# Optimization experiments

Measured on AMD Instinct MI355X. Metric: run time of the kernel, lower is better.

Reference implementation:

```python
import jax, jax.numpy as jnp
import numpy as np

N, D, DFF, H, L = 98280, 192, 384, 8, 36
S = N // L  # 2730 sets per partition
HD = D // H
EPS = 1e-5


def _ln(x, g, b):
    m = x.mean(-1, keepdims=True)
    v = ((x - m) ** 2).mean(-1, keepdims=True)
    return (x - m) * jax.lax.rsqrt(v + EPS) * g + b


def _mha(q, k, v, Wqkv, bqkv, Wo, bo, mask):
    # q,k,v: (S, L, D); mask: (S, L), True = padded key
    Wq, Wk, Wv = jnp.split(Wqkv, 3, axis=0)
    bq, bk, bv = jnp.split(bqkv, 3)
    qh = (q @ Wq.T + bq).reshape(S, L, H, HD)
    kh = (k @ Wk.T + bk).reshape(S, L, H, HD)
    vh = (v @ Wv.T + bv).reshape(S, L, H, HD)
    scores = jnp.einsum('slhd,smhd->shlm', qh, kh) / np.sqrt(HD).astype(np.float32)
    scores = jnp.where(mask[:, None, None, :], -1e9, scores)
    attn = jax.nn.softmax(scores, axis=-1)
    out = jnp.einsum('shlm,smhd->slhd', attn, vh).reshape(S, L, D)
    return out @ Wo.T + bo


def _layer(x, pos, inds, mask, Wqkv, bqkv, Wo, bo, W1, b1, W2, b2,
           g1, be1, g2, be2, gn, bn):
    identity = x
    sf = x[inds]                 # gather voxels into sets: (S, L, D)
    qk = sf + pos[inds]          # pos added to q and k only (value = sf)
    src2 = _mha(qk, qk, sf, Wqkv, bqkv, Wo, bo, mask)
    flat = inds.reshape(-1)
    # torch.unique(return_inverse) + flip + scatter == take FIRST occurrence
    # of each voxel id; .at[].min is deterministic under duplicates.
    perm = jnp.full((N,), flat.shape[0], jnp.int32).at[flat].min(
        jnp.arange(flat.shape[0], dtype=jnp.int32))
    src2 = src2.reshape(-1, D)[perm]   # scatter back: (N, D)
    x = _ln(x + src2, g1, be1)
    ff = jnp.maximum(x @ W1.T + b1, 0.0) @ W2.T + b2
    x = _ln(x + ff, g2, be2)
    return _ln(x + identity, gn, bn)   # DSVT_EncoderLayer residual norm


def reference(src, inds0, inds1, mask0, mask1, pos0, pos1,
              Wqkv, bqkv, Wo, bo, W1, b1, W2, b2,
              g1, be1, g2, be2, gn, bn, block_id):
    inds = (inds0, inds1)
    masks = (mask0, mask1)
    pos = (pos0, pos1)
    out = src
    for i in range(2):  # two set partitions within the shift (shift_id = block_id % 2)
        out = _layer(out, pos[i], inds[i], masks[i],
                     Wqkv[i], bqkv[i], Wo[i], bo[i],
                     W1[i], b1[i], W2[i], b2[i],
                     g1[i], be1[i], g2[i], be2[i], gn[i], bn[i])
    return out


def setup_inputs():
    key = jax.random.key(0)
    ks = jax.random.split(key, 16)
    sd = 0.02
    return {
        "src": jax.random.normal(ks[0], (N, D), jnp.float32),
        "inds0": jax.random.permutation(ks[1], N).reshape(S, L).astype(jnp.int32),
        "inds1": jax.random.permutation(ks[2], N).reshape(S, L).astype(jnp.int32),
        "mask0": jnp.zeros((S, L), bool),
        "mask1": jnp.zeros((S, L), bool),
        "pos0": jax.random.normal(ks[3], (N, D), jnp.float32),
        "pos1": jax.random.normal(ks[4], (N, D), jnp.float32),
        "Wqkv": sd * jax.random.normal(ks[5], (2, 3 * D, D), jnp.float32),
        "bqkv": jnp.zeros((2, 3 * D), jnp.float32),
        "Wo": sd * jax.random.normal(ks[6], (2, D, D), jnp.float32),
        "bo": jnp.zeros((2, D), jnp.float32),
        "W1": sd * jax.random.normal(ks[7], (2, DFF, D), jnp.float32),
        "b1": jnp.zeros((2, DFF), jnp.float32),
        "W2": sd * jax.random.normal(ks[8], (2, D, DFF), jnp.float32),
        "b2": jnp.zeros((2, D), jnp.float32),
        "g1": jnp.ones((2, D), jnp.float32),
        "be1": jnp.zeros((2, D), jnp.float32),
        "g2": jnp.ones((2, D), jnp.float32),
        "be2": jnp.zeros((2, D), jnp.float32),
        "gn": jnp.ones((2, D), jnp.float32),
        "bn": jnp.zeros((2, D), jnp.float32),
        "block_id": 0,
    }
```

## Files before the change

### kernel.cpp

```cpp
#include <hip/hip_runtime.h>
#include <stdint.h>

#define NVOX   98280
#define S_SETS 2730
#define L_SET  36
#define D_MODEL 192
#define D_FF    384
#define N_HEADS 8
#define H_DIM   24

using s16x8 = __attribute__((ext_vector_type(8))) short;
using s16x4 = __attribute__((ext_vector_type(4))) short;
using f32x4 = __attribute__((ext_vector_type(4))) float;

__device__ __forceinline__ float bf2f(unsigned short h) {
    unsigned u = ((unsigned)h) << 16;
    return __builtin_bit_cast(float, u);
}
__device__ __forceinline__ unsigned short f2bf(float f) {
    unsigned u = __builtin_bit_cast(unsigned, f);
    u += 0x7FFF + ((u >> 16) & 1);
    return (unsigned short)(u >> 16);
}

__global__ __launch_bounds__(256)
void convert_f32_bf16(const float* __restrict__ src, short* __restrict__ dst, int n)
{
    int i = blockIdx.x * 256 + threadIdx.x;
    if (i < n) dst[i] = (short)f2bf(src[i]);
}

__global__ __launch_bounds__(256)
void gather_kernel(const float* __restrict__ x, const float* __restrict__ pos,
                   const int* __restrict__ inds,
                   short* __restrict__ qk, short* __restrict__ sf)
{
    int f = blockIdx.x * 4 + (threadIdx.x >> 6);
    int lane = threadIdx.x & 63;
    if (lane >= 48) return;
    int v = inds[f];
    float4 a = *(const float4*)(x + (size_t)v * D_MODEL + lane * 4);
    float4 p = *(const float4*)(pos + (size_t)v * D_MODEL + lane * 4);
    s16x4 q, s;
    q[0] = (short)f2bf(a.x + p.x); q[1] = (short)f2bf(a.y + p.y);
    q[2] = (short)f2bf(a.z + p.z); q[3] = (short)f2bf(a.w + p.w);
    s[0] = (short)f2bf(a.x); s[1] = (short)f2bf(a.y);
    s[2] = (short)f2bf(a.z); s[3] = (short)f2bf(a.w);
    *(s16x4*)(qk + (size_t)f * D_MODEL + lane * 4) = q;
    *(s16x4*)(sf + (size_t)f * D_MODEL + lane * 4) = s;
}

__global__ __launch_bounds__(512, 4)
void qkv_direct(const short* __restrict__ qk, const short* __restrict__ sf,
                const short* __restrict__ W, const float* __restrict__ bias,
                short* __restrict__ C, int n)
{
    __shared__ char Bs[36864];
    const int bx = blockIdx.x;
    const int sec = bx >> 1, half = bx & 1;
    const int colOff = sec * 192 + half * 96;
    const short* Ap = (sec == 2) ? sf : qk;
    const short* Wp = W + (size_t)colOff * 192;
    const int rowBase = blockIdx.y * 128;
    const int tid = threadIdx.x;

    #pragma unroll
    for (int t = tid; t < 2304; t += 512) {
        int row = t / 24, c8 = t % 24;
        s16x8 v = *(const s16x8*)(Wp + (size_t)row * 192 + c8 * 8);
        *(s16x8*)(Bs + row * 384 + ((c8 * 16) ^ ((row & 7) << 4))) = v;
    }
    __syncthreads();

    const int wid = tid >> 6, lane = tid & 63;
    const int lr = lane & 15, kb = lane >> 4;
    const int arow = rowBase + wid * 16 + lr;
    const bool rv = arow < n;
    const short* Arow = Ap + (size_t)arow * 192 + kb * 8;

    f32x4 acc[6] = {};
    #pragma unroll
    for (int ks = 0; ks < 6; ++ks) {
        s16x8 a = {};
        if (rv) a = *(const s16x8*)(Arow + ks * 32);
        s16x8 b[6];
        #pragma unroll
        for (int fj = 0; fj < 6; ++fj) {
            int row = fj * 16 + lr;
            b[fj] = *(const s16x8*)(Bs + row * 384 + ((ks * 64 + kb * 16) ^ ((row & 7) << 4)));
        }
        #pragma unroll
        for (int fj = 0; fj < 6; ++fj)
            acc[fj] = __builtin_amdgcn_mfma_f32_16x16x32_bf16(a, b[fj], acc[fj], 0, 0, 0);
    }
    #pragma unroll
    for (int fj = 0; fj < 6; ++fj) {
        int col = colOff + fj * 16 + lr;
        float bv = bias[col];
        #pragma unroll
        for (int r = 0; r < 4; ++r) {
            int grow = rowBase + wid * 16 + kb * 4 + r;
            if (grow < n)
                C[(size_t)grow * 576 + col] = (short)f2bf(acc[fj][r] + bv);
        }
    }
}

__global__ __launch_bounds__(64)
void attn_mfma(const short* __restrict__ qkv, const unsigned char* __restrict__ mask,
               short* __restrict__ attn_out)
{
    const int s = blockIdx.x >> 3;
    const int h = blockIdx.x & 7;
    __shared__ short Pl[48 * 64];
    __shared__ short Vt[32 * 64];
    char* Pb = (char*)Pl;
    char* Vb = (char*)Vt;
    const int lane = threadIdx.x;
    const int lr = lane & 15, g = lane >> 4;

    #pragma unroll
    for (int i = 0; i < 6; ++i)
        *(s16x8*)(Pl + i * 512 + lane * 8) = (s16x8){};
    #pragma unroll
    for (int i = 0; i < 4; ++i)
        *(s16x8*)(Vt + i * 512 + lane * 8) = (s16x8){};
    if (lane < L_SET) {
        const short* vrow = qkv + (size_t)(s * L_SET + lane) * 576 + 384 + h * H_DIM;
        #pragma unroll
        for (int j = 0; j < 3; ++j) {
            s16x8 v = *(const s16x8*)(vrow + j * 8);
            #pragma unroll
            for (int e = 0; e < 8; ++e) {
                int d = j * 8 + e;
                *(short*)(Vb + d * 128 + ((lane * 2) ^ ((d & 7) << 4))) = v[e];
            }
        }
    }

    s16x8 qa[3], kb[3];
    #pragma unroll
    for (int t = 0; t < 3; ++t) {
        int rr = t * 16 + lr;
        qa[t] = (s16x8){};
        kb[t] = (s16x8){};
        if (rr < L_SET && g < 3) {
            const short* base = qkv + (size_t)(s * L_SET + rr) * 576 + h * H_DIM + g * 8;
            qa[t] = *(const s16x8*)(base);
            kb[t] = *(const s16x8*)(base + 192);
        }
    }
    f32x4 sc[3][3] = {};
    #pragma unroll
    for (int mt = 0; mt < 3; ++mt)
        #pragma unroll
        for (int nt = 0; nt < 3; ++nt)
            sc[mt][nt] = __builtin_amdgcn_mfma_f32_16x16x32_bf16(qa[mt], kb[nt], sc[mt][nt], 0, 0, 0);

    const float scale = 0.20412414523193154f;
    bool colmask[3];
    #pragma unroll
    for (int nt = 0; nt < 3; ++nt) {
        int m = nt * 16 + lr;
        colmask[nt] = (m >= L_SET) || (mask[(size_t)s * L_SET + (m < L_SET ? m : 0)] != 0);
    }
    #pragma unroll
    for (int mt = 0; mt < 3; ++mt) {
        #pragma unroll
        for (int r = 0; r < 4; ++r) {
            float v[3], ev[3];
            #pragma unroll
            for (int nt = 0; nt < 3; ++nt)
                v[nt] = colmask[nt] ? -1e9f : sc[mt][nt][r] * scale;
            float mx = fmaxf(fmaxf(v[0], v[1]), v[2]);
            #pragma unroll
            for (int off = 1; off < 16; off <<= 1) mx = fmaxf(mx, __shfl_xor(mx, off, 64));
            float sm = 0.f;
            #pragma unroll
            for (int nt = 0; nt < 3; ++nt) { ev[nt] = __expf(v[nt] - mx); sm += ev[nt]; }
            #pragma unroll
            for (int off = 1; off < 16; off <<= 1) sm += __shfl_xor(sm, off, 64);
            float rinv = 1.f / sm;
            int q = mt * 16 + g * 4 + r;
            #pragma unroll
            for (int nt = 0; nt < 3; ++nt) {
                int m = nt * 16 + lr;
                *(short*)(Pb + q * 128 + ((m * 2) ^ ((q & 7) << 4))) =
                    (short)f2bf(ev[nt] * rinv);
            }
        }
    }

    f32x4 o[3][2] = {};
    #pragma unroll
    for (int ks = 0; ks < 2; ++ks) {
        s16x8 pa[3], vb[2];
        #pragma unroll
        for (int mt = 0; mt < 3; ++mt) {
            int row = mt * 16 + lr;
            pa[mt] = *(const s16x8*)(Pb + row * 128 + ((ks * 64 + g * 16) ^ ((row & 7) << 4)));
        }
        #pragma unroll
        for (int nt = 0; nt < 2; ++nt) {
            int row = nt * 16 + lr;
            vb[nt] = *(const s16x8*)(Vb + row * 128 + ((ks * 64 + g * 16) ^ ((row & 7) << 4)));
        }
        #pragma unroll
        for (int mt = 0; mt < 3; ++mt)
            #pragma unroll
            for (int nt = 0; nt < 2; ++nt)
                o[mt][nt] = __builtin_amdgcn_mfma_f32_16x16x32_bf16(pa[mt], vb[nt], o[mt][nt], 0, 0, 0);
    }

    #pragma unroll
    for (int mt = 0; mt < 3; ++mt) {
        #pragma unroll
        for (int nt = 0; nt < 2; ++nt) {
            #pragma unroll
            for (int r = 0; r < 4; ++r) {
                int q = mt * 16 + g * 4 + r;
                int d = nt * 16 + lr;
                if (q < L_SET && d < H_DIM)
                    attn_out[(size_t)(s * L_SET + q) * D_MODEL + h * H_DIM + d] =
                        (short)f2bf(o[mt][nt][r]);
            }
        }
    }
}

__device__ __forceinline__ float wave_sum64(float v) {
    #pragma unroll
    for (int off = 32; off > 0; off >>= 1) v += __shfl_xor(v, off, 64);
    return v;
}

__global__ __launch_bounds__(512)
void wo_ln1(const short* __restrict__ attnb, const short* __restrict__ Wo,
            const float* __restrict__ bo, const int* __restrict__ inds,
            const float* __restrict__ xin,
            const float* __restrict__ g1, const float* __restrict__ be1,
            short* __restrict__ x1, int n)
{
    extern __shared__ char pool[];
    char* As = pool;
    char* Bs = pool + 49152;
    float* Cf = (float*)pool;
    const int rowBase = blockIdx.x * 128;
    const int tid = threadIdx.x;

    #pragma unroll
    for (int t = tid; t < 3072; t += 512) {
        int row = t / 24, c8 = t % 24;
        int grow = rowBase + row;
        s16x8 v = {};
        if (grow < n) v = *(const s16x8*)(attnb + (size_t)grow * 192 + c8 * 8);
        *(s16x8*)(As + row * 384 + ((c8 * 16) ^ ((row & 7) << 4))) = v;
    }
    #pragma unroll
    for (int t = tid; t < 4608; t += 512) {
        int row = t / 24, c8 = t % 24;
        s16x8 v = *(const s16x8*)(Wo + (size_t)row * 192 + c8 * 8);
        *(s16x8*)(Bs + row * 384 + ((c8 * 16) ^ ((row & 7) << 4))) = v;
    }
    __syncthreads();

    const int wid = tid >> 6, lane = tid & 63;
    const int lr = lane & 15, kb = lane >> 4;
    const int wm = wid & 3, wn = wid >> 2;
    f32x4 acc[2][6] = {};
    #pragma unroll
    for (int ks = 0; ks < 6; ++ks) {
        s16x8 a[2], b[6];
        #pragma unroll
        for (int fi = 0; fi < 2; ++fi) {
            int row = wm * 32 + fi * 16 + lr;
            a[fi] = *(const s16x8*)(As + row * 384 + ((ks * 64 + kb * 16) ^ ((row & 7) << 4)));
        }
        #pragma unroll
        for (int fj = 0; fj < 6; ++fj) {
            int row = wn * 96 + fj * 16 + lr;
            b[fj] = *(const s16x8*)(Bs + row * 384 + ((ks * 64 + kb * 16) ^ ((row & 7) << 4)));
        }
        #pragma unroll
        for (int fi = 0; fi < 2; ++fi)
            #pragma unroll
            for (int fj = 0; fj < 6; ++fj)
                acc[fi][fj] = __builtin_amdgcn_mfma_f32_16x16x32_bf16(a[fi], b[fj], acc[fi][fj], 0, 0, 0);
    }
    __syncthreads();
    #pragma unroll
    for (int fj = 0; fj < 6; ++fj) {
        int col = wn * 96 + fj * 16 + lr;
        float bv = bo[col];
        #pragma unroll
        for (int fi = 0; fi < 2; ++fi)
            #pragma unroll
            for (int r = 0; r < 4; ++r) {
                int row = wm * 32 + fi * 16 + kb * 4 + r;
                Cf[row * 192 + col] = acc[fi][fj][r] + bv;
            }
    }
    __syncthreads();

    int vv[16];
    #pragma unroll
    for (int i = 0; i < 16; ++i) {
        int f = rowBase + wid * 16 + i;
        vv[i] = (f < n) ? inds[f] : 0;
    }
    float4 xr[16];
    #pragma unroll
    for (int i = 0; i < 16; ++i)
        xr[i] = (lane < 48) ? *(const float4*)(xin + (size_t)vv[i] * D_MODEL + lane * 4)
                            : make_float4(0.f, 0.f, 0.f, 0.f);
    float4 gv = (lane < 48) ? *(const float4*)(g1 + lane * 4) : make_float4(0,0,0,0);
    float4 bv = (lane < 48) ? *(const float4*)(be1 + lane * 4) : make_float4(0,0,0,0);
    #pragma unroll
    for (int i = 0; i < 16; ++i) {
        int r = wid * 16 + i;
        int f = rowBase + r;
        float4 t = make_float4(0.f, 0.f, 0.f, 0.f);
        if (lane < 48) {
            float4 c4 = *(const float4*)&Cf[r * 192 + lane * 4];
            t.x = c4.x + xr[i].x; t.y = c4.y + xr[i].y;
            t.z = c4.z + xr[i].z; t.w = c4.w + xr[i].w;
        }
        float mean = wave_sum64(t.x + t.y + t.z + t.w) * (1.f / 192.f);
        float ss   = wave_sum64(t.x*t.x + t.y*t.y + t.z*t.z + t.w*t.w) * (1.f / 192.f);
        float inv = rsqrtf(ss - mean * mean + 1e-5f);
        if (lane < 48 && f < n) {
            s16x4 o;
            o[0] = (short)f2bf((t.x - mean) * inv * gv.x + bv.x);
            o[1] = (short)f2bf((t.y - mean) * inv * gv.y + bv.y);
            o[2] = (short)f2bf((t.z - mean) * inv * gv.z + bv.z);
            o[3] = (short)f2bf((t.w - mean) * inv * gv.w + bv.w);
            *(s16x4*)(x1 + (size_t)vv[i] * D_MODEL + lane * 4) = o;
        }
    }
}

__global__ __launch_bounds__(512)
void ffn_fused(const short* __restrict__ x1, const short* __restrict__ W1,
               const float* __restrict__ b1, const short* __restrict__ W2,
               const float* __restrict__ b2, const float* __restrict__ xin,
               const float* __restrict__ g2, const float* __restrict__ be2,
               const float* __restrict__ gn, const float* __restrict__ bn,
               float* __restrict__ outp, int n)
{
    extern __shared__ char pool[];
    char* Ax  = pool;
    char* W1c = pool + 49152;
    char* W2c = pool + 86016;
    char* Hc  = pool + 125952;
    float* Cf = (float*)(pool + 49152);
    const int rowBase = blockIdx.x * 128;
    const int tid = threadIdx.x;
    const int wid = tid >> 6, lane = tid & 63;
    const int lr = lane & 15, kb = lane >> 4;
    const int wm = wid & 3, wn = wid >> 2;

    #pragma unroll
    for (int t = tid; t < 3072; t += 512) {
        int row = t / 24, c8 = t % 24;
        int grow = rowBase + row;
        s16x8 v = {};
        if (grow < n) v = *(const s16x8*)(x1 + (size_t)grow * 192 + c8 * 8);
        *(s16x8*)(Ax + row * 384 + ((c8 * 16) ^ ((row & 7) << 4))) = v;
    }

    f32x4 acc2[2][6] = {};
    for (int c = 0; c < 4; ++c) {
        __syncthreads();
        #pragma unroll
        for (int t = tid; t < 2304; t += 512) {
            int row = t / 24, c8 = t % 24;
            s16x8 v = *(const s16x8*)(W1 + (size_t)(c * 96 + row) * 192 + c8 * 8);
            *(s16x8*)(W1c + row * 384 + ((c8 * 16) ^ ((row & 7) << 4))) = v;
        }
        #pragma unroll
        for (int t = tid; t < 2304; t += 512) {
            int row = t / 12, c8 = t % 12;
            s16x8 v = *(const s16x8*)(W2 + (size_t)row * 384 + c * 96 + c8 * 8);
            *(s16x8*)(W2c + row * 208 + c8 * 16) = v;
        }
        __syncthreads();
        f32x4 acc1[2][3] = {};
        #pragma unroll
        for (int ks = 0; ks < 6; ++ks) {
            s16x8 a[2], b[3];
            #pragma unroll
            for (int fi = 0; fi < 2; ++fi) {
                int row = wm * 32 + fi * 16 + lr;
                a[fi] = *(const s16x8*)(Ax + row * 384 + ((ks * 64 + kb * 16) ^ ((row & 7) << 4)));
            }
            #pragma unroll
            for (int fj = 0; fj < 3; ++fj) {
                int row = wn * 48 + fj * 16 + lr;
                b[fj] = *(const s16x8*)(W1c + row * 384 + ((ks * 64 + kb * 16) ^ ((row & 7) << 4)));
            }
            #pragma unroll
            for (int fi = 0; fi < 2; ++fi)
                #pragma unroll
                for (int fj = 0; fj < 3; ++fj)
                    acc1[fi][fj] = __builtin_amdgcn_mfma_f32_16x16x32_bf16(a[fi], b[fj], acc1[fi][fj], 0, 0, 0);
        }
        #pragma unroll
        for (int fj = 0; fj < 3; ++fj) {
            int col = wn * 48 + fj * 16 + lr;
            float b1v = b1[c * 96 + col];
            #pragma unroll
            for (int fi = 0; fi < 2; ++fi)
                #pragma unroll
                for (int r = 0; r < 4; ++r) {
                    int row = wm * 32 + fi * 16 + kb * 4 + r;
                    *(short*)(Hc + row * 208 + col * 2) =
                        (short)f2bf(fmaxf(acc1[fi][fj][r] + b1v, 0.f));
                }
        }
        __syncthreads();
        #pragma unroll
        for (int ks = 0; ks < 3; ++ks) {
            s16x8 a[2], b[6];
            #pragma unroll
            for (int fi = 0; fi < 2; ++fi) {
                int row = wm * 32 + fi * 16 + lr;
                a[fi] = *(const s16x8*)(Hc + row * 208 + ks * 64 + kb * 16);
            }
            #pragma unroll
            for (int fj = 0; fj < 6; ++fj) {
                int row = wn * 96 + fj * 16 + lr;
                b[fj] = *(const s16x8*)(W2c + row * 208 + ks * 64 + kb * 16);
            }
            #pragma unroll
            for (int fi = 0; fi < 2; ++fi)
                #pragma unroll
                for (int fj = 0; fj < 6; ++fj)
                    acc2[fi][fj] = __builtin_amdgcn_mfma_f32_16x16x32_bf16(a[fi], b[fj], acc2[fi][fj], 0, 0, 0);
        }
    }
    __syncthreads();
    #pragma unroll
    for (int fj = 0; fj < 6; ++fj) {
        int col = wn * 96 + fj * 16 + lr;
        float bv = b2[col];
        #pragma unroll
        for (int fi = 0; fi < 2; ++fi)
            #pragma unroll
            for (int r = 0; r < 4; ++r) {
                int row = wm * 32 + fi * 16 + kb * 4 + r;
                Cf[row * 192 + col] = acc2[fi][fj][r] + bv;
            }
    }
    __syncthreads();

    float4 xr[16];
    #pragma unroll
    for (int i = 0; i < 16; ++i) {
        int gvx = rowBase + wid * 16 + i;
        xr[i] = (lane < 48 && gvx < n)
              ? *(const float4*)(xin + (size_t)gvx * D_MODEL + lane * 4)
              : make_float4(0.f, 0.f, 0.f, 0.f);
    }
    float4 g2v = (lane < 48) ? *(const float4*)(g2 + lane * 4) : make_float4(0,0,0,0);
    float4 b2v = (lane < 48) ? *(const float4*)(be2 + lane * 4) : make_float4(0,0,0,0);
    float4 gnv = (lane < 48) ? *(const float4*)(gn + lane * 4) : make_float4(0,0,0,0);
    float4 bnv = (lane < 48) ? *(const float4*)(bn + lane * 4) : make_float4(0,0,0,0);
    #pragma unroll
    for (int i = 0; i < 16; ++i) {
        int r = wid * 16 + i;
        int gvx = rowBase + r;
        float4 t = make_float4(0.f, 0.f, 0.f, 0.f);
        if (lane < 48) {
            float4 f4 = *(const float4*)&Cf[r * 192 + lane * 4];
            int byteoff = r * 384 + (((lane >> 1) << 4) ^ ((r & 7) << 4)) + ((lane & 1) << 3);
            s16x4 xv = *(const s16x4*)(Ax + byteoff);
            t.x = f4.x + bf2f((unsigned short)xv[0]);
            t.y = f4.y + bf2f((unsigned short)xv[1]);
            t.z = f4.z + bf2f((unsigned short)xv[2]);
            t.w = f4.w + bf2f((unsigned short)xv[3]);
        }
        float m1 = wave_sum64(t.x + t.y + t.z + t.w) * (1.f / 192.f);
        float s1 = wave_sum64(t.x*t.x + t.y*t.y + t.z*t.z + t.w*t.w) * (1.f / 192.f);
        float i1 = rsqrtf(s1 - m1 * m1 + 1e-5f);
        float4 t2 = make_float4(0.f, 0.f, 0.f, 0.f);
        if (lane < 48) {
            t2.x = (t.x - m1) * i1 * g2v.x + b2v.x + xr[i].x;
            t2.y = (t.y - m1) * i1 * g2v.y + b2v.y + xr[i].y;
            t2.z = (t.z - m1) * i1 * g2v.z + b2v.z + xr[i].z;
            t2.w = (t.w - m1) * i1 * g2v.w + b2v.w + xr[i].w;
        }
        float m2 = wave_sum64(t2.x + t2.y + t2.z + t2.w) * (1.f / 192.f);
        float s2 = wave_sum64(t2.x*t2.x + t2.y*t2.y + t2.z*t2.z + t2.w*t2.w) * (1.f / 192.f);
        float i2 = rsqrtf(s2 - m2 * m2 + 1e-5f);
        if (lane < 48 && gvx < n) {
            float4 o;
            o.x = (t2.x - m2) * i2 * gnv.x + bnv.x;
            o.y = (t2.y - m2) * i2 * gnv.y + bnv.y;
            o.z = (t2.z - m2) * i2 * gnv.z + bnv.z;
            o.w = (t2.w - m2) * i2 * gnv.w + bnv.w;
            *(float4*)(outp + (size_t)gvx * D_MODEL + lane * 4) = o;
        }
    }
}

extern "C" void kernel_launch(void* const* d_in, const int* in_sizes, int n_in,
                              void* d_out, int out_size, void* d_ws, size_t ws_size,
                              hipStream_t stream)
{
    (void)in_sizes; (void)n_in; (void)out_size;
    const int N = NVOX;
    const float* src = (const float*)d_in[0];
    const int* inds[2] = {(const int*)d_in[1], (const int*)d_in[2]};
    const unsigned char* mask[2] = {(const unsigned char*)d_in[3], (const unsigned char*)d_in[4]};
    const float* pos[2] = {(const float*)d_in[5], (const float*)d_in[6]};
    const float* Wqkv = (const float*)d_in[7];
    const float* bqkv = (const float*)d_in[8];
    const float* Wo   = (const float*)d_in[9];
    const float* bo   = (const float*)d_in[10];
    const float* W1   = (const float*)d_in[11];
    const float* b1   = (const float*)d_in[12];
    const float* W2   = (const float*)d_in[13];
    const float* b2   = (const float*)d_in[14];
    const float* g1   = (const float*)d_in[15];
    const float* be1  = (const float*)d_in[16];
    const float* g2   = (const float*)d_in[17];
    const float* be2  = (const float*)d_in[18];
    const float* gn   = (const float*)d_in[19];
    const float* bn   = (const float*)d_in[20];

    float* out = (float*)d_out;
    short* wsS = (short*)d_ws;

    const size_t NE = (size_t)N * D_MODEL;
    short* wqkv_b = wsS;
    short* wo_b   = wsS + 221184;
    short* w1_b   = wsS + 294912;
    short* w2_b   = wsS + 442368;
    const size_t base = 1048576;
    short* qk    = wsS + base;
    short* sf    = qk + NE;
    short* qkvb  = sf + NE;
    short* attnb = qkvb + 3 * NE;
    short* x1    = attnb + NE;

    if (ws_size < (base + 7 * NE) * sizeof(short)) return;

    const dim3 blk(256);
    convert_f32_bf16<<<dim3(864), blk, 0, stream>>>(Wqkv, wqkv_b, 221184);
    convert_f32_bf16<<<dim3(288), blk, 0, stream>>>(Wo,   wo_b,   73728);
    convert_f32_bf16<<<dim3(576), blk, 0, stream>>>(W1,   w1_b,   147456);
    convert_f32_bf16<<<dim3(576), blk, 0, stream>>>(W2,   w2_b,   147456);

    const int RT = (N + 127) / 128;
    for (int i = 0; i < 2; ++i) {
        const float* xin = (i == 0) ? src : out;
        gather_kernel<<<dim3(24570), blk, 0, stream>>>(xin, pos[i], inds[i], qk, sf);
        qkv_direct<<<dim3(6, RT), dim3(512), 0, stream>>>(
            qk, sf, wqkv_b + (size_t)i * 110592, bqkv + i * 576, qkvb, N);
        attn_mfma<<<dim3(S_SETS * N_HEADS), dim3(64), 0, stream>>>(qkvb, mask[i], attnb);
        wo_ln1<<<dim3(RT), dim3(512), 122880, stream>>>(
            attnb, wo_b + (size_t)i * 36864, bo + i * 192, inds[i], xin,
            g1 + i * 192, be1 + i * 192, x1, N);
        ffn_fused<<<dim3(RT), dim3(512), 152576, stream>>>(
            x1, w1_b + (size_t)i * 73728, b1 + i * 384, w2_b + (size_t)i * 73728,
            b2 + i * 192, xin, g2 + i * 192, be2 + i * 192,
            gn + i * 192, bn + i * 192, out, N);
    }
}
```

Measured before the change: 790.1 us.

## Restructure Wo+LN1 and FFN kernels so each wave owns full output rows

Both post-attention kernels are rewritten to use 256-thread blocks in which each wave computes all 192 output columns for 32 rows. Weights are read straight from global memory (relying on cache) instead of being staged in LDS, and the A tile for Wo is also read directly. LayerNorm runs on the MFMA accumulators in registers with 16-lane shuffle reductions, removing the LDS round trip and several barriers. In exchange it raises register pressure (24 accumulator tiles plus temporaries), issues many narrow scalar global loads and stores for the residual and outputs, and re-reads weights per wave.

```diff
diff --git a/kernel.cpp b/kernel.cpp
--- a/kernel.cpp
+++ b/kernel.cpp
@@ -228,277 +228,210 @@
     }
 }
 
-__device__ __forceinline__ float wave_sum64(float v) {
-    #pragma unroll
-    for (int off = 32; off > 0; off >>= 1) v += __shfl_xor(v, off, 64);
-    return v;
-}
-
-__global__ __launch_bounds__(512)
-void wo_ln1(const short* __restrict__ attnb, const short* __restrict__ Wo,
-            const float* __restrict__ bo, const int* __restrict__ inds,
-            const float* __restrict__ xin,
-            const float* __restrict__ g1, const float* __restrict__ be1,
-            short* __restrict__ x1, int n)
-{
-    extern __shared__ char pool[];
-    char* As = pool;
-    char* Bs = pool + 49152;
-    float* Cf = (float*)pool;
+__global__ __launch_bounds__(256)
+void wo_wave(const short* __restrict__ attnb, const short* __restrict__ Wo,
+             const float* __restrict__ bo, const int* __restrict__ inds,
+             const float* __restrict__ xin,
+             const float* __restrict__ g1, const float* __restrict__ be1,
+             short* __restrict__ x1, int n)
+{
     const int rowBase = blockIdx.x * 128;
     const int tid = threadIdx.x;
-
-    #pragma unroll
-    for (int t = tid; t < 3072; t += 512) {
-        int row = t / 24, c8 = t % 24;
-        int grow = rowBase + row;
-        s16x8 v = {};
-        if (grow < n) v = *(const s16x8*)(attnb + (size_t)grow * 192 + c8 * 8);
-        *(s16x8*)(As + row * 384 + ((c8 * 16) ^ ((row & 7) << 4))) = v;
-    }
-    #pragma unroll
-    for (int t = tid; t < 4608; t += 512) {
-        int row = t / 24, c8 = t % 24;
-        s16x8 v = *(const s16x8*)(Wo + (size_t)row * 192 + c8 * 8);
-        *(s16x8*)(Bs + row * 384 + ((c8 * 16) ^ ((row & 7) << 4))) = v;
-    }
-    __syncthreads();
-
-    const int wid = tid >> 6, lane = tid & 63;
+    const int w = tid >> 6, lane = tid & 63;
     const int lr = lane & 15, kb = lane >> 4;
-    const int wm = wid & 3, wn = wid >> 2;
-    f32x4 acc[2][6] = {};
+
+    f32x4 acc[2][12] = {};
     #pragma unroll
     for (int ks = 0; ks < 6; ++ks) {
-        s16x8 a[2], b[6];
+        s16x8 a[2], b[12];
         #pragma unroll
         for (int fi = 0; fi < 2; ++fi) {
-            int row = wm * 32 + fi * 16 + lr;
-            a[fi] = *(const s16x8*)(As + row * 384 + ((ks * 64 + kb * 16) ^ ((row & 7) << 4)));
-        }
-        #pragma unroll
-        for (int fj = 0; fj < 6; ++fj) {
-            int row = wn * 96 + fj * 16 + lr;
-            b[fj] = *(const s16x8*)(Bs + row * 384 + ((ks * 64 + kb * 16) ^ ((row & 7) << 4)));
-        }
+            int arow = rowBase + w * 32 + fi * 16 + lr;
+            a[fi] = (s16x8){};
+            if (arow < n)
+                a[fi] = *(const s16x8*)(attnb + (size_t)arow * 192 + ks * 32 + kb * 8);
+        }
+        #pragma unroll
+        for (int fj = 0; fj < 12; ++fj)
+            b[fj] = *(const s16x8*)(Wo + (size_t)(fj * 16 + lr) * 192 + ks * 32 + kb * 8);
         #pragma unroll
         for (int fi = 0; fi < 2; ++fi)
             #pragma unroll
-            for (int fj = 0; fj < 6; ++fj)
+            for (int fj = 0; fj < 12; ++fj)
                 acc[fi][fj] = __builtin_amdgcn_mfma_f32_16x16x32_bf16(a[fi], b[fj], acc[fi][fj], 0, 0, 0);
     }
-    __syncthreads();
-    #pragma unroll
-    for (int fj = 0; fj < 6; ++fj) {
-        int col = wn * 96 + fj * 16 + lr;
-        float bv = bo[col];
-        #pragma unroll
-        for (int fi = 0; fi < 2; ++fi)
-            #pragma unroll
-            for (int r = 0; r < 4; ++r) {
-                int row = wm * 32 + fi * 16 + kb * 4 + r;
-                Cf[row * 192 + col] = acc[fi][fj][r] + bv;
-            }
-    }
-    __syncthreads();
-
-    int vv[16];
-    #pragma unroll
-    for (int i = 0; i < 16; ++i) {
-        int f = rowBase + wid * 16 + i;
-        vv[i] = (f < n) ? inds[f] : 0;
-    }
-    float4 xr[16];
-    #pragma unroll
-    for (int i = 0; i < 16; ++i)
-        xr[i] = (lane < 48) ? *(const float4*)(xin + (size_t)vv[i] * D_MODEL + lane * 4)
-                            : make_float4(0.f, 0.f, 0.f, 0.f);
-    float4 gv = (lane < 48) ? *(const float4*)(g1 + lane * 4) : make_float4(0,0,0,0);
-    float4 bv = (lane < 48) ? *(const float4*)(be1 + lane * 4) : make_float4(0,0,0,0);
-    #pragma unroll
-    for (int i = 0; i < 16; ++i) {
-        int r = wid * 16 + i;
-        int f = rowBase + r;
-        float4 t = make_float4(0.f, 0.f, 0.f, 0.f);
-        if (lane < 48) {
-            float4 c4 = *(const float4*)&Cf[r * 192 + lane * 4];
-            t.x = c4.x + xr[i].x; t.y = c4.y + xr[i].y;
-            t.z = c4.z + xr[i].z; t.w = c4.w + xr[i].w;
-        }
-        float mean = wave_sum64(t.x + t.y + t.z + t.w) * (1.f / 192.f);
-        float ss   = wave_sum64(t.x*t.x + t.y*t.y + t.z*t.z + t.w*t.w) * (1.f / 192.f);
-        float inv = rsqrtf(ss - mean * mean + 1e-5f);
-        if (lane < 48 && f < n) {
-            s16x4 o;
-            o[0] = (short)f2bf((t.x - mean) * inv * gv.x + bv.x);
-            o[1] = (short)f2bf((t.y - mean) * inv * gv.y + bv.y);
-            o[2] = (short)f2bf((t.z - mean) * inv * gv.z + bv.z);
-            o[3] = (short)f2bf((t.w - mean) * inv * gv.w + bv.w);
-            *(s16x4*)(x1 + (size_t)vv[i] * D_MODEL + lane * 4) = o;
-        }
-    }
-}
-
-__global__ __launch_bounds__(512)
-void ffn_fused(const short* __restrict__ x1, const short* __restrict__ W1,
-               const float* __restrict__ b1, const short* __restrict__ W2,
-               const float* __restrict__ b2, const float* __restrict__ xin,
-               const float* __restrict__ g2, const float* __restrict__ be2,
-               const float* __restrict__ gn, const float* __restrict__ bn,
-               float* __restrict__ outp, int n)
-{
-    extern __shared__ char pool[];
-    char* Ax  = pool;
-    char* W1c = pool + 49152;
-    char* W2c = pool + 86016;
-    char* Hc  = pool + 125952;
-    float* Cf = (float*)(pool + 49152);
+
+    float boc[12], g1c[12], be1c[12];
+    #pragma unroll
+    for (int fj = 0; fj < 12; ++fj) {
+        int col = fj * 16 + lr;
+        boc[fj] = bo[col]; g1c[fj] = g1[col]; be1c[fj] = be1[col];
+    }
+    #pragma unroll
+    for (int fi = 0; fi < 2; ++fi) {
+        #pragma unroll
+        for (int r = 0; r < 4; ++r) {
+            int f = rowBase + w * 32 + fi * 16 + kb * 4 + r;
+            bool valid = f < n;
+            int v = valid ? inds[f] : 0;
+            float t[12];
+            float s = 0.f, sq = 0.f;
+            #pragma unroll
+            for (int fj = 0; fj < 12; ++fj) {
+                int col = fj * 16 + lr;
+                float xi = valid ? xin[(size_t)v * D_MODEL + col] : 0.f;
+                float tv = acc[fi][fj][r] + boc[fj] + xi;
+                t[fj] = tv; s += tv; sq += tv * tv;
+            }
+            #pragma unroll
+            for (int off = 1; off < 16; off <<= 1) {
+                s  += __shfl_xor(s, off, 64);
+                sq += __shfl_xor(sq, off, 64);
+            }
+            float m = s * (1.f / 192.f);
+            float iv = rsqrtf(sq * (1.f / 192.f) - m * m + 1e-5f);
+            if (valid) {
+                #pragma unroll
+                for (int fj = 0; fj < 12; ++fj) {
+                    int col = fj * 16 + lr;
+                    x1[(size_t)v * D_MODEL + col] =
+                        (short)f2bf((t[fj] - m) * iv * g1c[fj] + be1c[fj]);
+                }
+            }
+        }
+    }
+}
+
+__global__ __launch_bounds__(256)
+void ffn_wave(const short* __restrict__ x1, const short* __restrict__ W1,
+              const float* __restrict__ b1, const short* __restrict__ W2,
+              const float* __restrict__ b2, const float* __restrict__ xin,
+              const float* __restrict__ g2, const float* __restrict__ be2,
+              const float* __restrict__ gn, const float* __restrict__ bn,
+              float* __restrict__ outp, int n)
+{
+    __shared__ char Ax[49152];
+    __shared__ char Hc[26624];
     const int rowBase = blockIdx.x * 128;
     const int tid = threadIdx.x;
-    const int wid = tid >> 6, lane = tid & 63;
+    const int w = tid >> 6, lane = tid & 63;
     const int lr = lane & 15, kb = lane >> 4;
-    const int wm = wid & 3, wn = wid >> 2;
-
-    #pragma unroll
-    for (int t = tid; t < 3072; t += 512) {
+
+    #pragma unroll
+    for (int t = tid; t < 3072; t += 256) {
         int row = t / 24, c8 = t % 24;
         int grow = rowBase + row;
         s16x8 v = {};
         if (grow < n) v = *(const s16x8*)(x1 + (size_t)grow * 192 + c8 * 8);
         *(s16x8*)(Ax + row * 384 + ((c8 * 16) ^ ((row & 7) << 4))) = v;
     }
-
-    f32x4 acc2[2][6] = {};
+    __syncthreads();
+
+    f32x4 acc2[2][12] = {};
     for (int c = 0; c < 4; ++c) {
-        __syncthreads();
-        #pragma unroll
-        for (int t = tid; t < 2304; t += 512) {
-            int row = t / 24, c8 = t % 24;
-            s16x8 v = *(const s16x8*)(W1 + (size_t)(c * 96 + row) * 192 + c8 * 8);
-            *(s16x8*)(W1c + row * 384 + ((c8 * 16) ^ ((row & 7) << 4))) = v;
-        }
-        #pragma unroll
-        for (int t = tid; t < 2304; t += 512) {
-            int row = t / 12, c8 = t % 12;
-            s16x8 v = *(const s16x8*)(W2 + (size_t)row * 384 + c * 96 + c8 * 8);
-            *(s16x8*)(W2c + row * 208 + c8 * 16) = v;
-        }
-        __syncthreads();
-        f32x4 acc1[2][3] = {};
+        f32x4 acc1[2][6] = {};
         #pragma unroll
         for (int ks = 0; ks < 6; ++ks) {
-            s16x8 a[2], b[3];
+            s16x8 a[2], b[6];
             #pragma unroll
             for (int fi = 0; fi < 2; ++fi) {
-                int row = wm * 32 + fi * 16 + lr;
+                int row = w * 32 + fi * 16 + lr;
                 a[fi] = *(const s16x8*)(Ax + row * 384 + ((ks * 64 + kb * 16) ^ ((row & 7) << 4)));
             }
             #pragma unroll
-            for (int fj = 0; fj < 3; ++fj) {
-                int row = wn * 48 + fj * 16 + lr;
-                b[fj] = *(const s16x8*)(W1c + row * 384 + ((ks * 64 + kb * 16) ^ ((row & 7) << 4)));
-            }
+            for (int fj = 0; fj < 6; ++fj)
+                b[fj] = *(const s16x8*)(W1 + (size_t)(c * 96 + fj * 16 + lr) * 192 + ks * 32 + kb * 8);
             #pragma unroll
             for (int fi = 0; fi < 2; ++fi)
                 #pragma unroll
-                for (int fj = 0; fj < 3; ++fj)
+                for (int fj = 0; fj < 6; ++fj)
                     acc1[fi][fj] = __builtin_amdgcn_mfma_f32_16x16x32_bf16(a[fi], b[fj], acc1[fi][fj], 0, 0, 0);
         }
         #pragma unroll
-        for (int fj = 0; fj < 3; ++fj) {
-            int col = wn * 48 + fj * 16 + lr;
+        for (int fj = 0; fj < 6; ++fj) {
+            int col = fj * 16 + lr;
             float b1v = b1[c * 96 + col];
             #pragma unroll
             for (int fi = 0; fi < 2; ++fi)
                 #pragma unroll
                 for (int r = 0; r < 4; ++r) {
-                    int row = wm * 32 + fi * 16 + kb * 4 + r;
+                    int row = w * 32 + fi * 16 + kb * 4 + r;
                     *(short*)(Hc + row * 208 + col * 2) =
                         (short)f2bf(fmaxf(acc1[fi][fj][r] + b1v, 0.f));
                 }
         }
-        __syncthreads();
         #pragma unroll
         for (int ks = 0; ks < 3; ++ks) {
-            s16x8 a[2], b[6];
+            s16x8 a[2], b[12];
             #pragma unroll
             for (int fi = 0; fi < 2; ++fi) {
-                int row = wm * 32 + fi * 16 + lr;
+                int row = w * 32 + fi * 16 + lr;
                 a[fi] = *(const s16x8*)(Hc + row * 208 + ks * 64 + kb * 16);
             }
             #pragma unroll
-            for (int fj = 0; fj < 6; ++fj) {
-                int row = wn * 96 + fj * 16 + lr;
-                b[fj] = *(const s16x8*)(W2c + row * 208 + ks * 64 + kb * 16);
-            }
+            for (int fj = 0; fj < 12; ++fj)
+                b[fj] = *(const s16x8*)(W2 + (size_t)(fj * 16 + lr) * 384 + c * 96 + ks * 32 + kb * 8);
             #pragma unroll
             for (int fi = 0; fi < 2; ++fi)
                 #pragma unroll
-                for (int fj = 0; fj < 6; ++fj)
+                for (int fj = 0; fj < 12; ++fj)
                     acc2[fi][fj] = __builtin_amdgcn_mfma_f32_16x16x32_bf16(a[fi], b[fj], acc2[fi][fj], 0, 0, 0);
         }
     }
-    __syncthreads();
-    #pragma unroll
-    for (int fj = 0; fj < 6; ++fj) {
-        int col = wn * 96 + fj * 16 + lr;
-        float bv = b2[col];
-        #pragma unroll
-        for (int fi = 0; fi < 2; ++fi)
-            #pragma unroll
-            for (int r = 0; r < 4; ++r) {
-                int row = wm * 32 + fi * 16 + kb * 4 + r;
-                Cf[row * 192 + col] = acc2[fi][fj][r] + bv;
-            }
-    }
-    __syncthreads();
-
-    float4 xr[16];
-    #pragma unroll
-    for (int i = 0; i < 16; ++i) {
-        int gvx = rowBase + wid * 16 + i;
-        xr[i] = (lane < 48 && gvx < n)
-              ? *(const float4*)(xin + (size_t)gvx * D_MODEL + lane * 4)
-              : make_float4(0.f, 0.f, 0.f, 0.f);
-    }
-    float4 g2v = (lane < 48) ? *(const float4*)(g2 + lane * 4) : make_float4(0,0,0,0);
-    float4 b2v = (lane < 48) ? *(const float4*)(be2 + lane * 4) : make_float4(0,0,0,0);
-    float4 gnv = (lane < 48) ? *(const float4*)(gn + lane * 4) : make_float4(0,0,0,0);
-    float4 bnv = (lane < 48) ? *(const float4*)(bn + lane * 4) : make_float4(0,0,0,0);
-    #pragma unroll
-    for (int i = 0; i < 16; ++i) {
-        int r = wid * 16 + i;
-        int gvx = rowBase + r;
-        float4 t = make_float4(0.f, 0.f, 0.f, 0.f);
-        if (lane < 48) {
-            float4 f4 = *(const float4*)&Cf[r * 192 + lane * 4];
-            int byteoff = r * 384 + (((lane >> 1) << 4) ^ ((r & 7) << 4)) + ((lane & 1) << 3);
-            s16x4 xv = *(const s16x4*)(Ax + byteoff);
-            t.x = f4.x + bf2f((unsigned short)xv[0]);
-            t.y = f4.y + bf2f((unsigned short)xv[1]);
-            t.z = f4.z + bf2f((unsigned short)xv[2]);
-            t.w = f4.w + bf2f((unsigned short)xv[3]);
-        }
-        float m1 = wave_sum64(t.x + t.y + t.z + t.w) * (1.f / 192.f);
-        float s1 = wave_sum64(t.x*t.x + t.y*t.y + t.z*t.z + t.w*t.w) * (1.f / 192.f);
-        float i1 = rsqrtf(s1 - m1 * m1 + 1e-5f);
-        float4 t2 = make_float4(0.f, 0.f, 0.f, 0.f);
-        if (lane < 48) {
-            t2.x = (t.x - m1) * i1 * g2v.x + b2v.x + xr[i].x;
-            t2.y = (t.y - m1) * i1 * g2v.y + b2v.y + xr[i].y;
-            t2.z = (t.z - m1) * i1 * g2v.z + b2v.z + xr[i].z;
-            t2.w = (t.w - m1) * i1 * g2v.w + b2v.w + xr[i].w;
-        }
-        float m2 = wave_sum64(t2.x + t2.y + t2.z + t2.w) * (1.f / 192.f);
-        float s2 = wave_sum64(t2.x*t2.x + t2.y*t2.y + t2.z*t2.z + t2.w*t2.w) * (1.f / 192.f);
-        float i2 = rsqrtf(s2 - m2 * m2 + 1e-5f);
-        if (lane < 48 && gvx < n) {
-            float4 o;
-            o.x = (t2.x - m2) * i2 * gnv.x + bnv.x;
-            o.y = (t2.y - m2) * i2 * gnv.y + bnv.y;
-            o.z = (t2.z - m2) * i2 * gnv.z + bnv.z;
-            o.w = (t2.w - m2) * i2 * gnv.w + bnv.w;
-            *(float4*)(outp + (size_t)gvx * D_MODEL + lane * 4) = o;
+
+    float b2c[12], g2c[12], be2c[12], gnc[12], bnc[12];
+    #pragma unroll
+    for (int fj = 0; fj < 12; ++fj) {
+        int col = fj * 16 + lr;
+        b2c[fj] = b2[col]; g2c[fj] = g2[col]; be2c[fj] = be2[col];
+        gnc[fj] = gn[col]; bnc[fj] = bn[col];
+    }
+    #pragma unroll
+    for (int fi = 0; fi < 2; ++fi) {
+        #pragma unroll
+        for (int r = 0; r < 4; ++r) {
+            int row = w * 32 + fi * 16 + kb * 4 + r;
+            int gvx = rowBase + row;
+            bool valid = gvx < n;
+            float t[12];
+            float s = 0.f, sq = 0.f;
+            #pragma unroll
+            for (int fj = 0; fj < 12; ++fj) {
+                int col = fj * 16 + lr;
+                unsigned short xv = *(const unsigned short*)(Ax + row * 384 + ((col * 2) ^ ((row & 7) << 4)));
+                float tv = acc2[fi][fj][r] + b2c[fj] + bf2f(xv);
+                t[fj] = tv; s += tv; sq += tv * tv;
+            }
+            #pragma unroll
+            for (int off = 1; off < 16; off <<= 1) {
+                s  += __shfl_xor(s, off, 64);
+                sq += __shfl_xor(sq, off, 64);
+            }
+            float m1 = s * (1.f / 192.f);
+            float i1 = rsqrtf(sq * (1.f / 192.f) - m1 * m1 + 1e-5f);
+            float t2[12];
+            float s2 = 0.f, sq2 = 0.f;
+            #pragma unroll
+            for (int fj = 0; fj < 12; ++fj) {
+                int col = fj * 16 + lr;
+                float xi = valid ? xin[(size_t)gvx * D_MODEL + col] : 0.f;
+                float v2 = (t[fj] - m1) * i1 * g2c[fj] + be2c[fj] + xi;
+                t2[fj] = v2; s2 += v2; sq2 += v2 * v2;
+            }
+            #pragma unroll
+            for (int off = 1; off < 16; off <<= 1) {
+                s2  += __shfl_xor(s2, off, 64);
+                sq2 += __shfl_xor(sq2, off, 64);
+            }
+            float m2 = s2 * (1.f / 192.f);
+            float i2 = rsqrtf(sq2 * (1.f / 192.f) - m2 * m2 + 1e-5f);
+            if (valid) {
+                #pragma unroll
+                for (int fj = 0; fj < 12; ++fj) {
+                    int col = fj * 16 + lr;
+                    outp[(size_t)gvx * D_MODEL + col] = (t2[fj] - m2) * i2 * gnc[fj] + bnc[fj];
+                }
+            }
         }
     }
 }
@@ -558,10 +491,10 @@
         qkv_direct<<<dim3(6, RT), dim3(512), 0, stream>>>(
             qk, sf, wqkv_b + (size_t)i * 110592, bqkv + i * 576, qkvb, N);
         attn_mfma<<<dim3(S_SETS * N_HEADS), dim3(64), 0, stream>>>(qkvb, mask[i], attnb);
-        wo_ln1<<<dim3(RT), dim3(512), 122880, stream>>>(
+        wo_wave<<<dim3(RT), blk, 0, stream>>>(
             attnb, wo_b + (size_t)i * 36864, bo + i * 192, inds[i], xin,
             g1 + i * 192, be1 + i * 192, x1, N);
-        ffn_fused<<<dim3(RT), dim3(512), 152576, stream>>>(
+        ffn_wave<<<dim3(RT), blk, 0, stream>>>(
             x1, w1_b + (size_t)i * 73728, b1 + i * 384, w2_b + (size_t)i * 73728,
             b2 + i * 192, xin, g2 + i * 192, be2 + i * 192,
             gn + i * 192, bn + i * 192, out, N);
```

Measured after the change: 888.8 us. +12.5%, slower.
